# Kernel optimization log

Measured on AMD Instinct MI355X. Metric: run time of the kernel, lower is better.

## Reference

```python
import jax, jax.numpy as jnp
import numpy as np

DIM = 512
NUM_HEADS = 8
HEAD_DIM = DIM // NUM_HEADS
EPS = 1e-12  # F.normalize eps


def _l2norm(x):
    # F.normalize(x, dim=-1): x / max(||x||, eps)
    n = jnp.sqrt(jnp.sum(x * x, axis=-1, keepdims=True))
    return x / jnp.maximum(n, EPS)


def setup_inputs() -> dict:
    key = jax.random.key(0)
    ks = jax.random.split(key, 5)
    B, T, D = 4, 2048, DIM
    z = jax.random.normal(ks[0], (B, T, D), dtype=jnp.float32)
    t = jnp.zeros((1,), dtype=jnp.float32)  # unused ODE time
    omega = jax.random.normal(ks[1], (1, 1, D), dtype=jnp.float32) * 0.1
    # nn.Linear default init scale ~ U(-1/sqrt(fan_in), 1/sqrt(fan_in))
    s = 1.0 / np.sqrt(D)
    W_qk = jax.random.uniform(ks[2], (2 * D, D), jnp.float32, -s, s)
    W_out = jax.random.uniform(ks[3], (D, D), jnp.float32, -s, s)
    b_out = jax.random.uniform(ks[4], (D,), jnp.float32, -s, s)
    return {"t": t, "z": z, "omega": omega, "W_qk": W_qk, "W_out": W_out, "b_out": b_out}


def reference(t, z, omega, W_qk, W_out, b_out):
    B, T, D = z.shape
    H, hd = NUM_HEADS, HEAD_DIM
    qk = z @ W_qk.T                      # [B,T,2D]
    q, k = qk[..., :D], qk[..., D:]
    q = _l2norm(q.reshape(B, T, H, hd))  # [B,T,H,hd]
    k = _l2norm(k.reshape(B, T, H, hd))
    # coupling: [B,H,T,T]
    coupling = jnp.einsum("bqhd,bkhd->bhqk", q, k)
    interaction = jnp.sin(coupling)
    force = jnp.einsum("bhqk,bkhd->bqhd", interaction, k).reshape(B, T, D)
    return omega + force @ W_out.T + b_out
```

## Files before the change

### kernel.cpp

```cpp
#include <hip/hip_runtime.h>
#include <hip/hip_bf16.h>

typedef unsigned short u16;
typedef __attribute__((ext_vector_type(8))) short short8;
typedef __attribute__((ext_vector_type(4))) short short4_;
typedef __attribute__((ext_vector_type(4))) float f32x4;
typedef __attribute__((ext_vector_type(4))) unsigned int uint4_;

#define B_ 4
#define T_ 2048
#define D_ 512
#define H_ 8
#define M_ (B_*T_)
#define INV2PI 0.15915494309189535f

__device__ u16   g_zb[M_*D_];
__device__ u16   g_wqk[2*D_*D_];
__device__ u16   g_wout[D_*D_];
__device__ float g_qk[(size_t)M_*2*D_];
__device__ u16   g_qb[M_*D_];
__device__ u16   g_kb[M_*D_];
__device__ u16   g_kT[(size_t)B_*H_*64*T_];
__device__ u16   g_force[M_*D_];

__device__ inline u16 f2bf(float f) {
  union { __hip_bfloat16 h; u16 u; } cv;
  cv.h = __float2bfloat16(f);
  return cv.u;
}

__device__ inline float sin2pi(float x) {
#if __has_builtin(__builtin_amdgcn_sinf)
  return __builtin_amdgcn_sinf(x);
#else
  return __sinf(x * 6.283185307179586f);
#endif
}

template<int WHICH>
__global__ void cvt_kernel(const float* __restrict__ in) {
  constexpr int n4 = (WHICH == 0) ? (M_*D_/4) : (WHICH == 1) ? (2*D_*D_/4) : (D_*D_/4);
  u16* out = (WHICH == 0) ? g_zb : (WHICH == 1) ? g_wqk : g_wout;
  int i = blockIdx.x*256 + threadIdx.x;
  if (i < n4) {
    f32x4 v = *(const f32x4*)(in + (size_t)i*4);
    short4_ o;
    o[0] = (short)f2bf(v[0]); o[1] = (short)f2bf(v[1]);
    o[2] = (short)f2bf(v[2]); o[3] = (short)f2bf(v[3]);
    *(short4_*)(out + (size_t)i*4) = o;
  }
}

template<int MODE>
__global__ __launch_bounds__(256, 2)
void gemm_bt(float* __restrict__ Cout, const float* __restrict__ add1,
             const float* __restrict__ add2) {
  constexpr int K = 512;
  constexpr int N = (MODE == 0) ? 1024 : 512;
  const u16* A  = (MODE == 0) ? g_zb  : g_force;
  const u16* Bt = (MODE == 0) ? g_wqk : g_wout;
  float* C = (MODE == 0) ? g_qk : Cout;

  __shared__ u16 As[128*72];
  __shared__ u16 Bs[128*72];
  const int m0 = blockIdx.x*128, n0 = blockIdx.y*128;
  const int t = threadIdx.x;
  const int w = t>>6, l = t&63;
  const int wr = (w>>1)*64, wc = (w&1)*64;
  const int lg = l>>4, li = l&15;
  const int srow = t>>3, scol = (t&7)*8;

  f32x4 acc[4][4] = {};

  for (int k0 = 0; k0 < K; k0 += 64) {
#pragma unroll
    for (int p = 0; p < 4; ++p) {
      int r = srow + p*32;
      *(short8*)&As[r*72 + scol] = *(const short8*)&A [(size_t)(m0+r)*K + k0 + scol];
      *(short8*)&Bs[r*72 + scol] = *(const short8*)&Bt[(size_t)(n0+r)*K + k0 + scol];
    }
    __syncthreads();
#pragma unroll
    for (int ks = 0; ks < 2; ++ks) {
      short8 af[4], bf[4];
#pragma unroll
      for (int i = 0; i < 4; ++i)
        af[i] = *(const short8*)&As[(wr + i*16 + li)*72 + ks*32 + lg*8];
#pragma unroll
      for (int j = 0; j < 4; ++j)
        bf[j] = *(const short8*)&Bs[(wc + j*16 + li)*72 + ks*32 + lg*8];
#pragma unroll
      for (int i = 0; i < 4; ++i)
#pragma unroll
        for (int j = 0; j < 4; ++j)
          acc[i][j] = __builtin_amdgcn_mfma_f32_16x16x32_bf16(af[i], bf[j], acc[i][j], 0, 0, 0);
    }
    __syncthreads();
  }

#pragma unroll
  for (int i = 0; i < 4; ++i) {
#pragma unroll
    for (int j = 0; j < 4; ++j) {
      int col = n0 + wc + j*16 + li;
      float badd = 0.f;
      if (MODE == 1) badd = add1[col] + add2[col];
#pragma unroll
      for (int r = 0; r < 4; ++r) {
        int row = m0 + wr + i*16 + lg*4 + r;
        C[(size_t)row*N + col] = acc[i][j][r] + badd;
      }
    }
  }
}

__global__ void normalize_qk_kernel() {
  int gid = blockIdx.x*256 + threadIdx.x;
  int l = gid & 63;
  int wv = gid >> 6;
  int row = wv >> 4, c = wv & 15;
  float x = g_qk[(size_t)row*1024 + c*64 + l];
  float s = x*x;
#pragma unroll
  for (int off = 32; off; off >>= 1) s += __shfl_xor(s, off);
  float scale = 1.0f / fmaxf(sqrtf(s), 1e-12f);
  if (c < 8) g_qb[(size_t)row*512 + c*64 + l]     = f2bf(x*scale*INV2PI);
  else       g_kb[(size_t)row*512 + (c-8)*64 + l] = f2bf(x*scale);
}

__global__ void transpose_k_kernel() {
  __shared__ u16 tile[64*72];
  const int t0 = blockIdx.x*64, bh = blockIdx.y;
  const int b = bh>>3, h = bh&7;
  const int t = threadIdx.x;
  {
    int r = t>>2, cs = (t&3)*16;
    const u16* src = g_kb + (size_t)(b*T_ + t0 + r)*D_ + h*64 + cs;
    *(short8*)&tile[r*72 + cs]     = *(const short8*)(src);
    *(short8*)&tile[r*72 + cs + 8] = *(const short8*)(src + 8);
  }
  __syncthreads();
  {
    int d = t>>2, ts = (t&3)*16;
    short8 o0, o1;
#pragma unroll
    for (int j = 0; j < 8; ++j) {
      o0[j] = (short)tile[(ts + j)*72 + d];
      o1[j] = (short)tile[(ts + 8 + j)*72 + d];
    }
    u16* dst = g_kT + ((size_t)bh*64 + d)*T_ + t0 + ts;
    *(short8*)(dst)     = o0;
    *(short8*)(dst + 8) = o1;
  }
}

__global__ __launch_bounds__(256, 2)
void kuramoto_attn_kernel() {
  __shared__ u16 Qs[128*72];
  __shared__ u16 Ks[128*72];
  __shared__ u16 KTs[64*136];
  const int qt = blockIdx.x;
  const int bh = blockIdx.y;
  const int b = bh>>3, h = bh&7;
  const int t = threadIdx.x;
  const int w = t>>6, l = t&63;
  const int lg = l>>4, li = l&15;

  {
    int r = t>>3, cs = (t&7)*8;
#pragma unroll
    for (int p = 0; p < 4; ++p) {
      int rr = r + p*32;
      *(short8*)&Qs[rr*72 + cs] =
        *(const short8*)&g_qb[(size_t)(b*T_ + qt*128 + rr)*D_ + h*64 + cs];
    }
  }

  f32x4 acc_o[2][4] = {};

  for (int kt = 0; kt < 16; ++kt) {
    __syncthreads();
    {
      int r = t>>3, cs = (t&7)*8;
#pragma unroll
      for (int p = 0; p < 4; ++p) {
        int rr = r + p*32;
        *(short8*)&Ks[rr*72 + cs] =
          *(const short8*)&g_kb[(size_t)(b*T_ + kt*128 + rr)*D_ + h*64 + cs];
      }
      int d = t>>4, ks2 = (t&15)*8;
#pragma unroll
      for (int p = 0; p < 4; ++p) {
        int dd = d + p*16;
        *(short8*)&KTs[dd*136 + ks2] =
          *(const short8*)&g_kT[((size_t)bh*64 + dd)*T_ + kt*128 + ks2];
      }
    }
    __syncthreads();

    f32x4 sacc[8][2] = {};
#pragma unroll
    for (int ks = 0; ks < 2; ++ks) {
      short8 af[8], bq[2];
#pragma unroll
      for (int i = 0; i < 8; ++i)
        af[i] = *(const short8*)&Ks[(i*16 + li)*72 + ks*32 + lg*8];
#pragma unroll
      for (int j = 0; j < 2; ++j)
        bq[j] = *(const short8*)&Qs[(w*32 + j*16 + li)*72 + ks*32 + lg*8];
#pragma unroll
      for (int i = 0; i < 8; ++i)
#pragma unroll
        for (int j = 0; j < 2; ++j)
          sacc[i][j] = __builtin_amdgcn_mfma_f32_16x16x32_bf16(af[i], bq[j], sacc[i][j], 0, 0, 0);
    }

    unsigned int pb2[8][2][2];
#pragma unroll
    for (int i = 0; i < 8; ++i)
#pragma unroll
      for (int j = 0; j < 2; ++j) {
        pb2[i][j][0] = (unsigned int)f2bf(sin2pi(sacc[i][j][0]))
                     | ((unsigned int)f2bf(sin2pi(sacc[i][j][1])) << 16);
        pb2[i][j][1] = (unsigned int)f2bf(sin2pi(sacc[i][j][2]))
                     | ((unsigned int)f2bf(sin2pi(sacc[i][j][3])) << 16);
      }

#pragma unroll
    for (int kks = 0; kks < 4; ++kks) {
      short8 apv[2];
#pragma unroll
      for (int j = 0; j < 2; ++j) {
        union { uint4_ u; short8 s; } cvt;
        cvt.u[0] = pb2[2*kks  ][j][0];
        cvt.u[1] = pb2[2*kks  ][j][1];
        cvt.u[2] = pb2[2*kks+1][j][0];
        cvt.u[3] = pb2[2*kks+1][j][1];
        apv[j] = cvt.s;
      }
#pragma unroll
      for (int di = 0; di < 4; ++di) {
        short4_ b1 = *(const short4_*)&KTs[(di*16 + li)*136 + kks*32 + lg*4];
        short4_ b2 = *(const short4_*)&KTs[(di*16 + li)*136 + kks*32 + 16 + lg*4];
        union { short4_ h[2]; short8 v; } bu;
        bu.h[0] = b1; bu.h[1] = b2;
#pragma unroll
        for (int j = 0; j < 2; ++j)
          acc_o[j][di] = __builtin_amdgcn_mfma_f32_16x16x32_bf16(apv[j], bu.v, acc_o[j][di], 0, 0, 0);
      }
    }
  }

#pragma unroll
  for (int j = 0; j < 2; ++j)
#pragma unroll
    for (int di = 0; di < 4; ++di)
#pragma unroll
      for (int r = 0; r < 4; ++r) {
        int row = b*T_ + qt*128 + w*32 + j*16 + lg*4 + r;
        int col = h*64 + di*16 + li;
        g_force[(size_t)row*D_ + col] = f2bf(acc_o[j][di][r]);
      }
}

extern "C" void kernel_launch(void* const* d_in, const int* in_sizes, int n_in,
                              void* d_out, int out_size, void* d_ws, size_t ws_size,
                              hipStream_t stream) {
  const float* z     = (const float*)d_in[1];
  const float* omega = (const float*)d_in[2];
  const float* Wqk   = (const float*)d_in[3];
  const float* Wout  = (const float*)d_in[4];
  const float* bout  = (const float*)d_in[5];
  float* out = (float*)d_out;

  cvt_kernel<0><<<M_*D_/4/256, 256, 0, stream>>>(z);
  cvt_kernel<1><<<2*D_*D_/4/256, 256, 0, stream>>>(Wqk);
  cvt_kernel<2><<<D_*D_/4/256, 256, 0, stream>>>(Wout);

  gemm_bt<0><<<dim3(M_/128, 1024/128), 256, 0, stream>>>(nullptr, nullptr, nullptr);

  normalize_qk_kernel<<<M_*16*64/256, 256, 0, stream>>>();

  transpose_k_kernel<<<dim3(T_/64, B_*H_), 256, 0, stream>>>();

  kuramoto_attn_kernel<<<dim3(T_/128, B_*H_), 256, 0, stream>>>();

  gemm_bt<1><<<dim3(M_/128, 512/128), 256, 0, stream>>>(out, omega, bout);
}
```

Measured before the change: 182.4 us.

## Fuse conversions and normalization into GEMMs, split attention over key halves

The three fp32-to-bf16 conversion kernels and the separate normalize kernel are removed. Conversion now happens while GEMM tiles are loaded, and L2 normalization with the 1/2π scale runs in the QK GEMM epilogue via a lane shuffle reduction, so the fp32 qk intermediate is never written. The attention kernel splits the key range in two, writing fp32 partial force into two buffers that the output GEMM sums on load. It also uses a remapped 1D grid, keeps Q fragments in registers instead of LDS, interleaves score and PV MFMAs per 32-key chunk, and reads a pre-permuted K transpose with single 16-byte LDS loads. The cost is extra fp32 partial-force traffic and redundant weight conversion in every GEMM block.

```diff
diff --git a/kernel.cpp b/kernel.cpp
--- a/kernel.cpp
+++ b/kernel.cpp
@@ -5,7 +5,6 @@
 typedef __attribute__((ext_vector_type(8))) short short8;
 typedef __attribute__((ext_vector_type(4))) short short4_;
 typedef __attribute__((ext_vector_type(4))) float f32x4;
-typedef __attribute__((ext_vector_type(4))) unsigned int uint4_;
 
 #define B_ 4
 #define T_ 2048
@@ -14,14 +13,11 @@
 #define M_ (B_*T_)
 #define INV2PI 0.15915494309189535f
 
-__device__ u16   g_zb[M_*D_];
-__device__ u16   g_wqk[2*D_*D_];
-__device__ u16   g_wout[D_*D_];
-__device__ float g_qk[(size_t)M_*2*D_];
 __device__ u16   g_qb[M_*D_];
 __device__ u16   g_kb[M_*D_];
-__device__ u16   g_kT[(size_t)B_*H_*64*T_];
-__device__ u16   g_force[M_*D_];
+__device__ u16   g_kTp[(size_t)B_*H_*64*T_];
+__device__ float g_fA[(size_t)M_*D_];
+__device__ float g_fB[(size_t)M_*D_];
 
 __device__ inline u16 f2bf(float f) {
   union { __hip_bfloat16 h; u16 u; } cv;
@@ -37,30 +33,25 @@
 #endif
 }
 
-template<int WHICH>
-__global__ void cvt_kernel(const float* __restrict__ in) {
-  constexpr int n4 = (WHICH == 0) ? (M_*D_/4) : (WHICH == 1) ? (2*D_*D_/4) : (D_*D_/4);
-  u16* out = (WHICH == 0) ? g_zb : (WHICH == 1) ? g_wqk : g_wout;
-  int i = blockIdx.x*256 + threadIdx.x;
-  if (i < n4) {
-    f32x4 v = *(const f32x4*)(in + (size_t)i*4);
-    short4_ o;
-    o[0] = (short)f2bf(v[0]); o[1] = (short)f2bf(v[1]);
-    o[2] = (short)f2bf(v[2]); o[3] = (short)f2bf(v[3]);
-    *(short4_*)(out + (size_t)i*4) = o;
-  }
+__device__ inline short8 cvt8(f32x4 a, f32x4 b) {
+  short8 o;
+  o[0]=(short)f2bf(a[0]); o[1]=(short)f2bf(a[1]); o[2]=(short)f2bf(a[2]); o[3]=(short)f2bf(a[3]);
+  o[4]=(short)f2bf(b[0]); o[5]=(short)f2bf(b[1]); o[6]=(short)f2bf(b[2]); o[7]=(short)f2bf(b[3]);
+  return o;
+}
+
+__device__ inline int perm5(int p) {
+  int lg = p >> 3, e = p & 7;
+  return (e < 4) ? lg*4 + e : 16 + lg*4 + (e & 3);
 }
 
 template<int MODE>
 __global__ __launch_bounds__(256, 2)
 void gemm_bt(float* __restrict__ Cout, const float* __restrict__ add1,
-             const float* __restrict__ add2) {
+             const float* __restrict__ add2, const float* __restrict__ Afp,
+             const float* __restrict__ Bfp) {
   constexpr int K = 512;
   constexpr int N = (MODE == 0) ? 1024 : 512;
-  const u16* A  = (MODE == 0) ? g_zb  : g_force;
-  const u16* Bt = (MODE == 0) ? g_wqk : g_wout;
-  float* C = (MODE == 0) ? g_qk : Cout;
-
   __shared__ u16 As[128*72];
   __shared__ u16 Bs[128*72];
   const int m0 = blockIdx.x*128, n0 = blockIdx.y*128;
@@ -76,8 +67,24 @@
 #pragma unroll
     for (int p = 0; p < 4; ++p) {
       int r = srow + p*32;
-      *(short8*)&As[r*72 + scol] = *(const short8*)&A [(size_t)(m0+r)*K + k0 + scol];
-      *(short8*)&Bs[r*72 + scol] = *(const short8*)&Bt[(size_t)(n0+r)*K + k0 + scol];
+      {
+        f32x4 b0 = *(const f32x4*)&Bfp[(size_t)(n0+r)*K + k0 + scol];
+        f32x4 b1 = *(const f32x4*)&Bfp[(size_t)(n0+r)*K + k0 + scol + 4];
+        *(short8*)&Bs[r*72 + scol] = cvt8(b0, b1);
+      }
+      if (MODE == 0) {
+        f32x4 a0 = *(const f32x4*)&Afp[(size_t)(m0+r)*K + k0 + scol];
+        f32x4 a1 = *(const f32x4*)&Afp[(size_t)(m0+r)*K + k0 + scol + 4];
+        *(short8*)&As[r*72 + scol] = cvt8(a0, a1);
+      } else {
+        size_t off = (size_t)(m0+r)*K + k0 + scol;
+        f32x4 a0 = *(const f32x4*)&g_fA[off];
+        f32x4 a1 = *(const f32x4*)&g_fA[off+4];
+        f32x4 c0 = *(const f32x4*)&g_fB[off];
+        f32x4 c1 = *(const f32x4*)&g_fB[off+4];
+        a0 += c0; a1 += c1;
+        *(short8*)&As[r*72 + scol] = cvt8(a0, a1);
+      }
     }
     __syncthreads();
 #pragma unroll
@@ -98,34 +105,42 @@
     __syncthreads();
   }
 
-#pragma unroll
-  for (int i = 0; i < 4; ++i) {
-#pragma unroll
-    for (int j = 0; j < 4; ++j) {
-      int col = n0 + wc + j*16 + li;
-      float badd = 0.f;
-      if (MODE == 1) badd = add1[col] + add2[col];
+  if (MODE == 0) {
+    const bool isq = (n0 < 512);
+    u16* dst = isq ? g_qb : g_kb;
+    const float qs = isq ? INV2PI : 1.0f;
+    const int nb = (isq ? n0 : n0 - 512) + wc;
+#pragma unroll
+    for (int i = 0; i < 4; ++i) {
 #pragma unroll
       for (int r = 0; r < 4; ++r) {
+        float s = 0.f;
+#pragma unroll
+        for (int j = 0; j < 4; ++j) s += acc[i][j][r]*acc[i][j][r];
+#pragma unroll
+        for (int off = 1; off < 16; off <<= 1) s += __shfl_xor(s, off);
+        float sc = qs / fmaxf(sqrtf(s), 1e-12f);
         int row = m0 + wr + i*16 + lg*4 + r;
-        C[(size_t)row*N + col] = acc[i][j][r] + badd;
-      }
-    }
-  }
-}
-
-__global__ void normalize_qk_kernel() {
-  int gid = blockIdx.x*256 + threadIdx.x;
-  int l = gid & 63;
-  int wv = gid >> 6;
-  int row = wv >> 4, c = wv & 15;
-  float x = g_qk[(size_t)row*1024 + c*64 + l];
-  float s = x*x;
-#pragma unroll
-  for (int off = 32; off; off >>= 1) s += __shfl_xor(s, off);
-  float scale = 1.0f / fmaxf(sqrtf(s), 1e-12f);
-  if (c < 8) g_qb[(size_t)row*512 + c*64 + l]     = f2bf(x*scale*INV2PI);
-  else       g_kb[(size_t)row*512 + (c-8)*64 + l] = f2bf(x*scale);
+#pragma unroll
+        for (int j = 0; j < 4; ++j)
+          dst[(size_t)row*D_ + nb + j*16 + li] = f2bf(acc[i][j][r]*sc);
+      }
+    }
+  } else {
+#pragma unroll
+    for (int i = 0; i < 4; ++i) {
+#pragma unroll
+      for (int j = 0; j < 4; ++j) {
+        int col = n0 + wc + j*16 + li;
+        float badd = add1[col] + add2[col];
+#pragma unroll
+        for (int r = 0; r < 4; ++r) {
+          int row = m0 + wr + i*16 + lg*4 + r;
+          Cout[(size_t)row*N + col] = acc[i][j][r] + badd;
+        }
+      }
+    }
+  }
 }
 
 __global__ void transpose_k_kernel() {
@@ -145,40 +160,41 @@
     short8 o0, o1;
 #pragma unroll
     for (int j = 0; j < 8; ++j) {
-      o0[j] = (short)tile[(ts + j)*72 + d];
-      o1[j] = (short)tile[(ts + 8 + j)*72 + d];
-    }
-    u16* dst = g_kT + ((size_t)bh*64 + d)*T_ + t0 + ts;
+      int p0 = ts + j, p1 = ts + 8 + j;
+      int s0 = (p0 & ~31) | perm5(p0 & 31);
+      int s1 = (p1 & ~31) | perm5(p1 & 31);
+      o0[j] = (short)tile[s0*72 + d];
+      o1[j] = (short)tile[s1*72 + d];
+    }
+    u16* dst = g_kTp + ((size_t)bh*64 + d)*T_ + t0 + ts;
     *(short8*)(dst)     = o0;
     *(short8*)(dst + 8) = o1;
   }
 }
 
-__global__ __launch_bounds__(256, 2)
+__global__ __launch_bounds__(256, 4)
 void kuramoto_attn_kernel() {
-  __shared__ u16 Qs[128*72];
   __shared__ u16 Ks[128*72];
   __shared__ u16 KTs[64*136];
-  const int qt = blockIdx.x;
-  const int bh = blockIdx.y;
-  const int b = bh>>3, h = bh&7;
+  const int wg  = blockIdx.x;
+  const int wgp = (wg & 7)*128 + (wg >> 3);
+  const int bh = wgp >> 5, qt = (wgp & 31) >> 1, kh = wgp & 1;
+  const int b = bh >> 3, h = bh & 7;
   const int t = threadIdx.x;
   const int w = t>>6, l = t&63;
   const int lg = l>>4, li = l&15;
 
-  {
-    int r = t>>3, cs = (t&7)*8;
-#pragma unroll
-    for (int p = 0; p < 4; ++p) {
-      int rr = r + p*32;
-      *(short8*)&Qs[rr*72 + cs] =
-        *(const short8*)&g_qb[(size_t)(b*T_ + qt*128 + rr)*D_ + h*64 + cs];
-    }
-  }
+  short8 bq[2][2];
+#pragma unroll
+  for (int ks = 0; ks < 2; ++ks)
+#pragma unroll
+    for (int j = 0; j < 2; ++j)
+      bq[ks][j] = *(const short8*)&g_qb[(size_t)(b*T_ + qt*128 + w*32 + j*16 + li)*D_
+                                        + h*64 + ks*32 + lg*8];
 
   f32x4 acc_o[2][4] = {};
 
-  for (int kt = 0; kt < 16; ++kt) {
+  for (int kt = kh*8; kt < kh*8 + 8; ++kt) {
     __syncthreads();
     {
       int r = t>>3, cs = (t&7)*8;
@@ -193,64 +209,45 @@
       for (int p = 0; p < 4; ++p) {
         int dd = d + p*16;
         *(short8*)&KTs[dd*136 + ks2] =
-          *(const short8*)&g_kT[((size_t)bh*64 + dd)*T_ + kt*128 + ks2];
-      }
-    }
-    __syncthreads();
-
-    f32x4 sacc[8][2] = {};
-#pragma unroll
-    for (int ks = 0; ks < 2; ++ks) {
-      short8 af[8], bq[2];
-#pragma unroll
-      for (int i = 0; i < 8; ++i)
-        af[i] = *(const short8*)&Ks[(i*16 + li)*72 + ks*32 + lg*8];
-#pragma unroll
-      for (int j = 0; j < 2; ++j)
-        bq[j] = *(const short8*)&Qs[(w*32 + j*16 + li)*72 + ks*32 + lg*8];
-#pragma unroll
-      for (int i = 0; i < 8; ++i)
+          *(const short8*)&g_kTp[((size_t)bh*64 + dd)*T_ + kt*128 + ks2];
+      }
+    }
+    __syncthreads();
+
+#pragma unroll
+    for (int kkp = 0; kkp < 4; ++kkp) {
+      f32x4 sacc[2][2] = {};
+#pragma unroll
+      for (int ks = 0; ks < 2; ++ks) {
+        short8 af0 = *(const short8*)&Ks[((2*kkp  )*16 + li)*72 + ks*32 + lg*8];
+        short8 af1 = *(const short8*)&Ks[((2*kkp+1)*16 + li)*72 + ks*32 + lg*8];
+#pragma unroll
+        for (int j = 0; j < 2; ++j) {
+          sacc[0][j] = __builtin_amdgcn_mfma_f32_16x16x32_bf16(af0, bq[ks][j], sacc[0][j], 0,0,0);
+          sacc[1][j] = __builtin_amdgcn_mfma_f32_16x16x32_bf16(af1, bq[ks][j], sacc[1][j], 0,0,0);
+        }
+      }
+      short8 apv[2];
+#pragma unroll
+      for (int j = 0; j < 2; ++j) {
+        union { unsigned int u[4]; short8 s; } cv;
+        cv.u[0] = (unsigned)f2bf(sin2pi(sacc[0][j][0])) | ((unsigned)f2bf(sin2pi(sacc[0][j][1]))<<16);
+        cv.u[1] = (unsigned)f2bf(sin2pi(sacc[0][j][2])) | ((unsigned)f2bf(sin2pi(sacc[0][j][3]))<<16);
+        cv.u[2] = (unsigned)f2bf(sin2pi(sacc[1][j][0])) | ((unsigned)f2bf(sin2pi(sacc[1][j][1]))<<16);
+        cv.u[3] = (unsigned)f2bf(sin2pi(sacc[1][j][2])) | ((unsigned)f2bf(sin2pi(sacc[1][j][3]))<<16);
+        apv[j] = cv.s;
+      }
+#pragma unroll
+      for (int di = 0; di < 4; ++di) {
+        short8 bv = *(const short8*)&KTs[(di*16 + li)*136 + kkp*32 + lg*8];
 #pragma unroll
         for (int j = 0; j < 2; ++j)
-          sacc[i][j] = __builtin_amdgcn_mfma_f32_16x16x32_bf16(af[i], bq[j], sacc[i][j], 0, 0, 0);
-    }
-
-    unsigned int pb2[8][2][2];
-#pragma unroll
-    for (int i = 0; i < 8; ++i)
-#pragma unroll
-      for (int j = 0; j < 2; ++j) {
-        pb2[i][j][0] = (unsigned int)f2bf(sin2pi(sacc[i][j][0]))
-                     | ((unsigned int)f2bf(sin2pi(sacc[i][j][1])) << 16);
-        pb2[i][j][1] = (unsigned int)f2bf(sin2pi(sacc[i][j][2]))
-                     | ((unsigned int)f2bf(sin2pi(sacc[i][j][3])) << 16);
-      }
-
-#pragma unroll
-    for (int kks = 0; kks < 4; ++kks) {
-      short8 apv[2];
-#pragma unroll
-      for (int j = 0; j < 2; ++j) {
-        union { uint4_ u; short8 s; } cvt;
-        cvt.u[0] = pb2[2*kks  ][j][0];
-        cvt.u[1] = pb2[2*kks  ][j][1];
-        cvt.u[2] = pb2[2*kks+1][j][0];
-        cvt.u[3] = pb2[2*kks+1][j][1];
-        apv[j] = cvt.s;
-      }
-#pragma unroll
-      for (int di = 0; di < 4; ++di) {
-        short4_ b1 = *(const short4_*)&KTs[(di*16 + li)*136 + kks*32 + lg*4];
-        short4_ b2 = *(const short4_*)&KTs[(di*16 + li)*136 + kks*32 + 16 + lg*4];
-        union { short4_ h[2]; short8 v; } bu;
-        bu.h[0] = b1; bu.h[1] = b2;
-#pragma unroll
-        for (int j = 0; j < 2; ++j)
-          acc_o[j][di] = __builtin_amdgcn_mfma_f32_16x16x32_bf16(apv[j], bu.v, acc_o[j][di], 0, 0, 0);
-      }
-    }
-  }
-
+          acc_o[j][di] = __builtin_amdgcn_mfma_f32_16x16x32_bf16(apv[j], bv, acc_o[j][di], 0,0,0);
+      }
+    }
+  }
+
+  float* F = kh ? g_fB : g_fA;
 #pragma unroll
   for (int j = 0; j < 2; ++j)
 #pragma unroll
@@ -259,7 +256,7 @@
       for (int r = 0; r < 4; ++r) {
         int row = b*T_ + qt*128 + w*32 + j*16 + lg*4 + r;
         int col = h*64 + di*16 + li;
-        g_force[(size_t)row*D_ + col] = f2bf(acc_o[j][di][r]);
+        F[(size_t)row*D_ + col] = acc_o[j][di][r];
       }
 }
 
@@ -273,17 +270,8 @@
   const float* bout  = (const float*)d_in[5];
   float* out = (float*)d_out;
 
-  cvt_kernel<0><<<M_*D_/4/256, 256, 0, stream>>>(z);
-  cvt_kernel<1><<<2*D_*D_/4/256, 256, 0, stream>>>(Wqk);
-  cvt_kernel<2><<<D_*D_/4/256, 256, 0, stream>>>(Wout);
-
-  gemm_bt<0><<<dim3(M_/128, 1024/128), 256, 0, stream>>>(nullptr, nullptr, nullptr);
-
-  normalize_qk_kernel<<<M_*16*64/256, 256, 0, stream>>>();
-
+  gemm_bt<0><<<dim3(M_/128, 1024/128), 256, 0, stream>>>(nullptr, nullptr, nullptr, z, Wqk);
   transpose_k_kernel<<<dim3(T_/64, B_*H_), 256, 0, stream>>>();
-
-  kuramoto_attn_kernel<<<dim3(T_/128, B_*H_), 256, 0, stream>>>();
-
-  gemm_bt<1><<<dim3(M_/128, 512/128), 256, 0, stream>>>(out, omega, bout);
-}
+  kuramoto_attn_kernel<<<1024, 256, 0, stream>>>();
+  gemm_bt<1><<<dim3(M_/128, 512/128), 256, 0, stream>>>(out, omega, bout, nullptr, Wout);
+}
```

After: 168.8 us. 7.5% less time.
